# Performance work log

Hardware: AMD Instinct MI355X
Metric: run time of the kernel (lower is better)

## Reference

```python
import jax, jax.numpy as jnp
import numpy as np

B, T, E, H = 4, 2048, 1024, 16
D = E // H
SCALE = 1.0 / np.sqrt(D)


def setup_inputs() -> dict:
    key = jax.random.key(0)
    ks = jax.random.split(key, 5)
    s_in = 1.0 / np.sqrt(E)
    return {
        "x": jax.random.normal(ks[0], (B, T, E), dtype=jnp.float32),
        "W_qkv": jax.random.normal(ks[1], (E, 3 * E), dtype=jnp.float32) * s_in,
        "b_qkv": jax.random.normal(ks[2], (3 * E,), dtype=jnp.float32) * 0.02,
        "W_proj": jax.random.normal(ks[3], (E, E), dtype=jnp.float32) * s_in,
        "b_proj": jax.random.normal(ks[4], (E,), dtype=jnp.float32) * 0.02,
    }


def reference(x, W_qkv, b_qkv, W_proj, b_proj):
    Bx, Tx, _ = x.shape
    qkv = x @ W_qkv + b_qkv                      # [B, T, 3E]
    q, k, v = jnp.split(qkv, 3, axis=2)
    q = q.reshape(Bx, Tx, H, D)
    k = k.reshape(Bx, Tx, H, D)
    v = v.reshape(Bx, Tx, H, D)
    # scores [B, H, T, T]
    a = SCALE * jnp.einsum("bthd,bshd->bhts", q, k)
    causal = jnp.tril(jnp.ones((Tx, Tx), dtype=bool))
    a = jnp.where(causal, a, -jnp.inf)
    a = jax.nn.softmax(a, axis=-1)
    y = jnp.einsum("bhts,bshd->bthd", a, v).reshape(Bx, Tx, E)
    return y @ W_proj + b_proj
```

## Files before the change

### kernel.cpp

```cpp
#include <hip/hip_runtime.h>
#include <math.h>

#define Bn 4
#define Tn 2048
#define En 1024
#define Hn 16
#define Dn 64
#define RS2 (2 * En)
#define QSCALE 0.18033688f
#define SMAX 16.0f

typedef __attribute__((ext_vector_type(8))) short bfrag;
typedef __attribute__((ext_vector_type(4))) short sfrag4;
typedef __attribute__((ext_vector_type(4))) float ffrag;

__device__ __forceinline__ unsigned short f2bf(float f) {
    union { float f; unsigned int u; } v; v.f = f;
    unsigned int r = v.u + 0x7fffu + ((v.u >> 16) & 1u);
    return (unsigned short)(r >> 16);
}
__device__ __forceinline__ unsigned short f2bf_fast(float f) {
    union { float f; unsigned int u; } v; v.f = f;
    return (unsigned short)((v.u + 0x8000u) >> 16);
}

__device__ __forceinline__ void glds16(const unsigned short* g, unsigned short* l) {
    __builtin_amdgcn_global_load_lds(
        (const __attribute__((address_space(1))) unsigned int*)g,
        (__attribute__((address_space(3))) unsigned int*)l, 16, 0, 0);
}

#define VMCNT0() asm volatile("s_waitcnt vmcnt(0)" ::: "memory")
#define BAR()    __builtin_amdgcn_s_barrier()

__global__ __launch_bounds__(256) void f2bf_vec(const float* __restrict__ in,
                                                unsigned short* __restrict__ out, int n) {
    int i = (blockIdx.x * 256 + threadIdx.x) * 4;
    if (i >= n) return;
    float4 v = *(const float4*)(in + i);
    ushort4 o;
    o.x = f2bf(v.x); o.y = f2bf(v.y); o.z = f2bf(v.z); o.w = f2bf(v.w);
    *(ushort4*)(out + i) = o;
}

__global__ __launch_bounds__(256) void transpose_f2bf(const float* __restrict__ W,
                                                      unsigned short* __restrict__ Wt,
                                                      int K, int N) {
    __shared__ float s[64][65];
    const int kt = blockIdx.y * 64, nt = blockIdx.x * 64;
    const int tx = threadIdx.x & 15, ty = threadIdx.x >> 4;
#pragma unroll
    for (int i = 0; i < 4; ++i) {
        float4 v = *(const float4*)&W[(size_t)(kt + ty + i * 16) * N + nt + tx * 4];
        s[ty + i * 16][tx * 4 + 0] = v.x;
        s[ty + i * 16][tx * 4 + 1] = v.y;
        s[ty + i * 16][tx * 4 + 2] = v.z;
        s[ty + i * 16][tx * 4 + 3] = v.w;
    }
    __syncthreads();
#pragma unroll
    for (int i = 0; i < 4; ++i) {
        const int n = ty + i * 16;
        ushort4 o;
        o.x = f2bf(s[tx * 4 + 0][n]);
        o.y = f2bf(s[tx * 4 + 1][n]);
        o.z = f2bf(s[tx * 4 + 2][n]);
        o.w = f2bf(s[tx * 4 + 3][n]);
        *(ushort4*)&Wt[(size_t)(nt + n) * K + kt + tx * 4] = o;
    }
}

template <int OUT_BF16, int VSPLIT>
__global__ __launch_bounds__(256) void gemm_nt_mfma(
    const unsigned short* __restrict__ A, const unsigned short* __restrict__ Bt,
    const float* __restrict__ bias, void* __restrict__ Cv, int ldc,
    unsigned short* __restrict__ vt, int vstart,
    int M, int N, int K, int qcols, int gx)
{
    __shared__ __attribute__((aligned(16))) unsigned short As[2][128 * 64];
    __shared__ __attribute__((aligned(16))) unsigned short Bs[2][128 * 64];

    const int t = threadIdx.x;
    const int w = t >> 6, l = t & 63;
    const int wmt = (w & 1) * 4, wnt = (w >> 1) * 4;
    const int nl = l & 15, lq = l >> 4;
    const int r8 = l >> 3, c8 = l & 7;
    const int cs8 = c8 ^ r8;

    const int flat = blockIdx.x;
    const int xcd = flat & 7;
    const int g = flat >> 3;
    const int bx = g % gx;
    const int by = xcd * 8 + g / gx;
    const int m0 = by * 128, n0 = bx * 128;

    ffrag acc[4][4];
#pragma unroll
    for (int i = 0; i < 4; ++i)
#pragma unroll
        for (int j = 0; j < 4; ++j)
#pragma unroll
            for (int r = 0; r < 4; ++r) acc[i][j][r] = 0.f;

    const unsigned short* Ag = A  + (size_t)(m0 + r8) * K + cs8 * 8;
    const unsigned short* Bg = Bt + (size_t)(n0 + r8) * K + cs8 * 8;

    const int iters = K >> 6;

#pragma unroll
    for (int r = 0; r < 4; ++r) {
        const int i = w * 4 + r;
        glds16(Ag + (size_t)(i * 8) * K, &As[0][i * 512 + l * 8]);
        glds16(Bg + (size_t)(i * 8) * K, &Bs[0][i * 512 + l * 8]);
    }
    __syncthreads();

#pragma unroll 1
    for (int it = 0; it < iters; ++it) {
        const int cur = it & 1;
        if (it + 1 < iters) {
            const int kn = (it + 1) << 6;
#pragma unroll
            for (int r = 0; r < 4; ++r) {
                const int i = w * 4 + r;
                glds16(Ag + (size_t)(i * 8) * K + kn, &As[cur ^ 1][i * 512 + l * 8]);
                glds16(Bg + (size_t)(i * 8) * K + kn, &Bs[cur ^ 1][i * 512 + l * 8]);
            }
        }
#pragma unroll
        for (int ks = 0; ks < 2; ++ks) {
            bfrag af[4], bf[4];
#pragma unroll
            for (int i = 0; i < 4; ++i) {
                const int pos = ((ks * 4 + lq) ^ (nl & 7)) << 3;
                af[i] = *(const bfrag*)&As[cur][((wmt + i) * 16 + nl) * 64 + pos];
                bf[i] = *(const bfrag*)&Bs[cur][((wnt + i) * 16 + nl) * 64 + pos];
            }
#pragma unroll
            for (int i = 0; i < 4; ++i)
#pragma unroll
                for (int j = 0; j < 4; ++j)
                    acc[i][j] = __builtin_amdgcn_mfma_f32_16x16x32_bf16(af[i], bf[j], acc[i][j], 0, 0, 0);
        }
        VMCNT0();
        BAR();
    }

    const int orow = lq * 4, ocol = nl;
#pragma unroll
    for (int i = 0; i < 4; ++i) {
        const int gm = m0 + (wmt + i) * 16 + orow;
#pragma unroll
        for (int j = 0; j < 4; ++j) {
            const int gn = n0 + (wnt + j) * 16 + ocol;
            const float bs = bias[gn];
            if (VSPLIT && gn >= vstart) {
                const int vc = gn - vstart;
                const int b  = gm / Tn;
                const int tt = gm - b * Tn;
                ushort4 o;
                o.x = f2bf(acc[i][j][0] + bs);
                o.y = f2bf(acc[i][j][1] + bs);
                o.z = f2bf(acc[i][j][2] + bs);
                o.w = f2bf(acc[i][j][3] + bs);
                *(ushort4*)&vt[(size_t)(b * Hn * Dn + vc) * Tn + tt] = o;
            } else {
                const float sc = (qcols && gn < qcols) ? QSCALE : 1.f;
#pragma unroll
                for (int r = 0; r < 4; ++r) {
                    const float vv = (acc[i][j][r] + bs) * sc;
                    if (OUT_BF16)
                        ((unsigned short*)Cv)[(size_t)(gm + r) * ldc + gn] = f2bf(vv);
                    else
                        ((float*)Cv)[(size_t)(gm + r) * ldc + gn] = vv;
                }
            }
        }
    }
}

__global__ __launch_bounds__(256) void attn_mfma(
    const unsigned short* __restrict__ qkv,
    const unsigned short* __restrict__ vtg,
    unsigned short* __restrict__ yattn)
{
    __shared__ __attribute__((aligned(16))) unsigned short KT[128 * 64];
    __shared__ __attribute__((aligned(16))) unsigned short VT[64 * 128];

    const int t = threadIdx.x;
    const int w = t >> 6, l = t & 63;
    const int nl = l & 15, lq = l >> 4;
    const int flat = blockIdx.x;
    const int bh = flat & 63;
    const int qp = flat >> 6;
    const int b = bh >> 4, h = bh & 15;

    const unsigned short* qbase = qkv + (size_t)(b * Tn) * RS2 + h * Dn;
    const unsigned short* kbase = qbase + En;
    const unsigned short* vbase = vtg + (size_t)(bh * Dn) * Tn;
    unsigned short* yb = yattn + (size_t)(b * Tn) * En + h * Dn;

#pragma unroll 1
    for (int phase = 0; phase < 2; ++phase) {
        const int qt = phase ? (15 - qp) : qp;
        const int rowb = qt * 128 + w * 16;
        const int jmax = qt;

        bfrag qf[2][2];
#pragma unroll
        for (int sub = 0; sub < 2; ++sub)
#pragma unroll
            for (int ks = 0; ks < 2; ++ks)
                qf[sub][ks] = *(const bfrag*)(qbase + (size_t)(rowb + sub * 64 + nl) * RS2 + ks * 32 + lq * 8);

        ffrag Oa[2][4];
        float li[2];
#pragma unroll
        for (int sub = 0; sub < 2; ++sub) {
            li[sub] = 0.f;
#pragma unroll
            for (int dt = 0; dt < 4; ++dt)
#pragma unroll
                for (int r = 0; r < 4; ++r) Oa[sub][dt][r] = 0.f;
        }

        for (int j = 0; j <= jmax; ++j) {
            const int k0 = j << 7;
            __syncthreads();
#pragma unroll
            for (int r = 0; r < 4; ++r) {
                const int i = w * 4 + r;
                glds16(kbase + (size_t)(k0 + i * 8 + (l >> 3)) * RS2 + (((l & 7) ^ (l >> 3)) << 3),
                       &KT[i * 512 + l * 8]);
            }
#pragma unroll
            for (int r = 0; r < 4; ++r) {
                const int i = w * 4 + r;
                const int key = ((i & 3) << 2) + (l >> 4);
                glds16(vbase + (size_t)(i * 4 + (l >> 4)) * Tn + k0 + (((l & 15) ^ key) << 3),
                       &VT[i * 512 + l * 8]);
            }
            __syncthreads();

            bfrag pf[2][4];
#pragma unroll
            for (int cs = 0; cs < 4; ++cs) {
                const int n0 = cs * 2, n1 = cs * 2 + 1;
                const int pos0 = (lq ^ (nl & 7)) << 3;
                const int pos1 = ((4 + lq) ^ (nl & 7)) << 3;
                bfrag ka0 = *(const bfrag*)&KT[(n0 * 16 + nl) * 64 + pos0];
                bfrag kb0 = *(const bfrag*)&KT[(n0 * 16 + nl) * 64 + pos1];
                bfrag ka1 = *(const bfrag*)&KT[(n1 * 16 + nl) * 64 + pos0];
                bfrag kb1 = *(const bfrag*)&KT[(n1 * 16 + nl) * 64 + pos1];
#pragma unroll
                for (int sub = 0; sub < 2; ++sub) {
                    const int qrow = rowb + sub * 64 + nl;
                    ffrag z0, z1;
#pragma unroll
                    for (int r = 0; r < 4; ++r) { z0[r] = -SMAX; z1[r] = -SMAX; }
                    __builtin_amdgcn_s_setprio(1);
                    z0 = __builtin_amdgcn_mfma_f32_16x16x32_bf16(ka0, qf[sub][0], z0, 0, 0, 0);
                    z0 = __builtin_amdgcn_mfma_f32_16x16x32_bf16(kb0, qf[sub][1], z0, 0, 0, 0);
                    z1 = __builtin_amdgcn_mfma_f32_16x16x32_bf16(ka1, qf[sub][0], z1, 0, 0, 0);
                    z1 = __builtin_amdgcn_mfma_f32_16x16x32_bf16(kb1, qf[sub][1], z1, 0, 0, 0);
                    __builtin_amdgcn_s_setprio(0);
                    if (j == jmax) {
#pragma unroll
                        for (int r = 0; r < 4; ++r) {
                            if (k0 + n0 * 16 + lq * 4 + r > qrow) z0[r] = -INFINITY;
                            if (k0 + n1 * 16 + lq * 4 + r > qrow) z1[r] = -INFINITY;
                        }
                    }
#pragma unroll
                    for (int r = 0; r < 4; ++r) {
                        const float p0 = __builtin_amdgcn_exp2f(z0[r]);
                        const float p1 = __builtin_amdgcn_exp2f(z1[r]);
                        li[sub] += p0;
                        li[sub] += p1;
                        pf[sub][cs][r]     = (short)f2bf_fast(p0);
                        pf[sub][cs][4 + r] = (short)f2bf_fast(p1);
                    }
                }
            }

            __builtin_amdgcn_s_setprio(1);
#pragma unroll
            for (int cs = 0; cs < 4; ++cs) {
#pragma unroll
                for (int dt = 0; dt < 4; ++dt) {
                    const int d = dt * 16 + nl;
                    const int base = d * 128 + ((lq & 1) << 2);
                    const int cA = (((cs << 2) + (lq >> 1)) ^ nl) << 3;
                    const int cB = (((cs << 2) + 2 + (lq >> 1)) ^ nl) << 3;
                    sfrag4 va = *(const sfrag4*)&VT[base + cA];
                    sfrag4 vb = *(const sfrag4*)&VT[base + cB];
                    bfrag vf = __builtin_shufflevector(va, vb, 0, 1, 2, 3, 4, 5, 6, 7);
                    Oa[0][dt] = __builtin_amdgcn_mfma_f32_16x16x32_bf16(pf[0][cs], vf, Oa[0][dt], 0, 0, 0);
                    Oa[1][dt] = __builtin_amdgcn_mfma_f32_16x16x32_bf16(pf[1][cs], vf, Oa[1][dt], 0, 0, 0);
                }
            }
            __builtin_amdgcn_s_setprio(0);
        }

#pragma unroll
        for (int sub = 0; sub < 2; ++sub) {
            float ls = li[sub];
            ls += __shfl_xor(ls, 16, 64);
            ls += __shfl_xor(ls, 32, 64);
#pragma unroll
            for (int r = 0; r < 4; ++r) {
                const float lr = __shfl(ls, lq * 4 + r, 64);
                const float inv = 1.f / lr;
                const int row = rowb + sub * 64 + lq * 4 + r;
#pragma unroll
                for (int dt = 0; dt < 4; ++dt)
                    yb[(size_t)row * En + dt * 16 + nl] = f2bf(Oa[sub][dt][r] * inv);
            }
        }
    }
}

extern "C" void kernel_launch(void* const* d_in, const int* in_sizes, int n_in,
                              void* d_out, int out_size, void* d_ws, size_t ws_size,
                              hipStream_t stream)
{
    const float* x      = (const float*)d_in[0];
    const float* W_qkv  = (const float*)d_in[1];
    const float* b_qkv  = (const float*)d_in[2];
    const float* W_proj = (const float*)d_in[3];
    const float* b_proj = (const float*)d_in[4];
    float* out = (float*)d_out;

    const int M = Bn * Tn;
    char* ws = (char*)d_ws;
    unsigned short* xb   = (unsigned short*)ws; ws += (size_t)M * En * 2;
    unsigned short* Wqt  = (unsigned short*)ws; ws += (size_t)3 * En * En * 2;
    unsigned short* Wpt  = (unsigned short*)ws; ws += (size_t)En * En * 2;
    unsigned short* qkb  = (unsigned short*)ws; ws += (size_t)M * 2 * En * 2;
    unsigned short* vtg  = (unsigned short*)ws; ws += (size_t)M * En * 2;
    unsigned short* yb   = (unsigned short*)ws;

    f2bf_vec<<<(M * En / 4 + 255) / 256, 256, 0, stream>>>(x, xb, M * En);
    transpose_f2bf<<<dim3(3 * En / 64, En / 64), 256, 0, stream>>>(W_qkv, Wqt, En, 3 * En);
    transpose_f2bf<<<dim3(En / 64, En / 64), 256, 0, stream>>>(W_proj, Wpt, En, En);

    gemm_nt_mfma<1, 1><<<dim3((3 * En / 128) * (M / 128)), 256, 0, stream>>>(
        xb, Wqt, b_qkv, qkb, 2 * En, vtg, 2 * En, M, 3 * En, En, En, 3 * En / 128);

    attn_mfma<<<dim3(512), 256, 0, stream>>>(qkb, vtg, yb);

    gemm_nt_mfma<0, 0><<<dim3((En / 128) * (M / 128)), 256, 0, stream>>>(
        yb, Wpt, b_proj, out, En, nullptr, 1 << 30, M, En, En, 0, En / 128);
}
```

Before: 246.0 us.

## Double-buffer K/V tiles in LDS to overlap global loads with MFMA compute

Doubles the K and V shared-memory tiles and issues the async global-to-LDS load for the next key block before computing on the current one. A vmcnt wait and a barrier at the end of each iteration replace the two barriers around the load, so load latency can hide behind the QK and PV MFMAs. LDS use doubles to 64 KB per block, which may cut occupancy. The loop is also marked unroll 1.

After: 246.0 us. About the same (-0.0%).

```diff
diff --git a/kernel.cpp b/kernel.cpp
--- a/kernel.cpp
+++ b/kernel.cpp
@@ -184,8 +184,8 @@
     const unsigned short* __restrict__ vtg,
     unsigned short* __restrict__ yattn)
 {
-    __shared__ __attribute__((aligned(16))) unsigned short KT[128 * 64];
-    __shared__ __attribute__((aligned(16))) unsigned short VT[64 * 128];
+    __shared__ __attribute__((aligned(16))) unsigned short KT[2][128 * 64];
+    __shared__ __attribute__((aligned(16))) unsigned short VT[2][64 * 128];
 
     const int t = threadIdx.x;
     const int w = t >> 6, l = t & 63;
@@ -224,23 +224,35 @@
                 for (int r = 0; r < 4; ++r) Oa[sub][dt][r] = 0.f;
         }
 
+#define STAGE_KV(J, BUF)                                                                   \
+        {                                                                                  \
+            const int k0s = (J) << 7;                                                      \
+            _Pragma("unroll")                                                              \
+            for (int r = 0; r < 4; ++r) {                                                  \
+                const int i = w * 4 + r;                                                   \
+                glds16(kbase + (size_t)(k0s + i * 8 + (l >> 3)) * RS2 +                    \
+                           (((l & 7) ^ (l >> 3)) << 3),                                    \
+                       &KT[BUF][i * 512 + l * 8]);                                         \
+            }                                                                              \
+            _Pragma("unroll")                                                              \
+            for (int r = 0; r < 4; ++r) {                                                  \
+                const int i = w * 4 + r;                                                   \
+                const int key = ((i & 3) << 2) + (l >> 4);                                 \
+                glds16(vbase + (size_t)(i * 4 + (l >> 4)) * Tn + k0s +                     \
+                           (((l & 15) ^ key) << 3),                                        \
+                       &VT[BUF][i * 512 + l * 8]);                                         \
+            }                                                                              \
+        }
+
+        STAGE_KV(0, 0);
+        VMCNT0();
+        __syncthreads();
+
+#pragma unroll 1
         for (int j = 0; j <= jmax; ++j) {
+            const int cur = j & 1;
             const int k0 = j << 7;
-            __syncthreads();
-#pragma unroll
-            for (int r = 0; r < 4; ++r) {
-                const int i = w * 4 + r;
-                glds16(kbase + (size_t)(k0 + i * 8 + (l >> 3)) * RS2 + (((l & 7) ^ (l >> 3)) << 3),
-                       &KT[i * 512 + l * 8]);
-            }
-#pragma unroll
-            for (int r = 0; r < 4; ++r) {
-                const int i = w * 4 + r;
-                const int key = ((i & 3) << 2) + (l >> 4);
-                glds16(vbase + (size_t)(i * 4 + (l >> 4)) * Tn + k0 + (((l & 15) ^ key) << 3),
-                       &VT[i * 512 + l * 8]);
-            }
-            __syncthreads();
+            if (j < jmax) STAGE_KV(j + 1, cur ^ 1);
 
             bfrag pf[2][4];
 #pragma unroll
@@ -248,10 +260,10 @@
                 const int n0 = cs * 2, n1 = cs * 2 + 1;
                 const int pos0 = (lq ^ (nl & 7)) << 3;
                 const int pos1 = ((4 + lq) ^ (nl & 7)) << 3;
-                bfrag ka0 = *(const bfrag*)&KT[(n0 * 16 + nl) * 64 + pos0];
-                bfrag kb0 = *(const bfrag*)&KT[(n0 * 16 + nl) * 64 + pos1];
-                bfrag ka1 = *(const bfrag*)&KT[(n1 * 16 + nl) * 64 + pos0];
-                bfrag kb1 = *(const bfrag*)&KT[(n1 * 16 + nl) * 64 + pos1];
+                bfrag ka0 = *(const bfrag*)&KT[cur][(n0 * 16 + nl) * 64 + pos0];
+                bfrag kb0 = *(const bfrag*)&KT[cur][(n0 * 16 + nl) * 64 + pos1];
+                bfrag ka1 = *(const bfrag*)&KT[cur][(n1 * 16 + nl) * 64 + pos0];
+                bfrag kb1 = *(const bfrag*)&KT[cur][(n1 * 16 + nl) * 64 + pos1];
 #pragma unroll
                 for (int sub = 0; sub < 2; ++sub) {
                     const int qrow = rowb + sub * 64 + nl;
@@ -292,15 +304,19 @@
                     const int base = d * 128 + ((lq & 1) << 2);
                     const int cA = (((cs << 2) + (lq >> 1)) ^ nl) << 3;
                     const int cB = (((cs << 2) + 2 + (lq >> 1)) ^ nl) << 3;
-                    sfrag4 va = *(const sfrag4*)&VT[base + cA];
-                    sfrag4 vb = *(const sfrag4*)&VT[base + cB];
+                    sfrag4 va = *(const sfrag4*)&VT[cur][base + cA];
+                    sfrag4 vb = *(const sfrag4*)&VT[cur][base + cB];
                     bfrag vf = __builtin_shufflevector(va, vb, 0, 1, 2, 3, 4, 5, 6, 7);
                     Oa[0][dt] = __builtin_amdgcn_mfma_f32_16x16x32_bf16(pf[0][cs], vf, Oa[0][dt], 0, 0, 0);
                     Oa[1][dt] = __builtin_amdgcn_mfma_f32_16x16x32_bf16(pf[1][cs], vf, Oa[1][dt], 0, 0, 0);
                 }
             }
             __builtin_amdgcn_s_setprio(0);
-        }
+
+            VMCNT0();
+            __syncthreads();
+        }
+#undef STAGE_KV
 
 #pragma unroll
         for (int sub = 0; sub < 2; ++sub) {
```
